# Kernel tuning notes

Hardware: AMD Instinct MI355X
Metric: run time of the kernel (lower is better)

Reference implementation:

```python
import jax, jax.numpy as jnp
import numpy as np

D_MODEL = 1024
D_HEAD = 512
EPS = 1e-6


def setup_inputs() -> dict:
    key = jax.random.key(0)
    ks = jax.random.split(key, 12)
    s = 0.02
    B, T = 8, 2048
    return {
        "x": jax.random.normal(ks[0], (B, T, D_MODEL), dtype=jnp.float32),
        "norm_w": jnp.ones((D_MODEL,), dtype=jnp.float32),
        "Wq": jax.random.normal(ks[1], (D_HEAD, D_MODEL), dtype=jnp.float32) * s,
        "Wk": jax.random.normal(ks[2], (D_HEAD, D_MODEL), dtype=jnp.float32) * s,
        "Wv": jax.random.normal(ks[3], (D_HEAD, D_MODEL), dtype=jnp.float32) * s,
        "wi_w": jax.random.normal(ks[4], (1, D_MODEL), dtype=jnp.float32) * s,
        "wi_b": jnp.zeros((1,), dtype=jnp.float32),
        "wf_w": jax.random.normal(ks[5], (1, D_MODEL), dtype=jnp.float32) * s,
        "wf_b": jnp.zeros((1,), dtype=jnp.float32),
        "Wo": jax.random.normal(ks[6], (D_HEAD, D_MODEL), dtype=jnp.float32) * s,
        "bo": jnp.zeros((D_HEAD,), dtype=jnp.float32),
        "Wout": jax.random.normal(ks[7], (D_MODEL, D_HEAD), dtype=jnp.float32) * s,
    }


def _forward(x, norm_w, Wq, Wk, Wv, wi_w, wi_b, wf_w, wf_b, Wo, bo, Wout):
    B, T, d_model = x.shape
    d = Wq.shape[0]
    scale = 1.0 / jnp.sqrt(jnp.asarray(d, x.dtype))

    # RMSNorm (pre-norm)
    normed = x * jax.lax.rsqrt(jnp.mean(x * x, axis=-1, keepdims=True) + EPS) * norm_w

    # Precompute all per-timestep projections (vectorized over T)
    q = jnp.einsum('btm,dm->btd', normed, Wq) * scale  # (B,T,d)
    k = jnp.einsum('btm,dm->btd', normed, Wk) * scale
    v = jnp.einsum('btm,dm->btd', normed, Wv)
    zi = jnp.einsum('btm,m->bt', normed, wi_w[0]) + wi_b[0]  # (B,T)
    zf = jnp.einsum('btm,m->bt', normed, wf_w[0]) + wf_b[0]
    o = jax.nn.sigmoid(jnp.einsum('btm,dm->btd', normed, Wo) + bo)  # (B,T,d)

    # Time-major for scan
    qT = jnp.moveaxis(q, 1, 0)
    kT = jnp.moveaxis(k, 1, 0)
    vT = jnp.moveaxis(v, 1, 0)
    ziT = jnp.moveaxis(zi, 1, 0)
    zfT = jnp.moveaxis(zf, 1, 0)
    oT = jnp.moveaxis(o, 1, 0)

    C0 = jnp.zeros((B, d, d), x.dtype)
    n0 = jnp.zeros((B, d), x.dtype)
    m0 = jnp.full((B,), -jnp.inf, x.dtype)

    def step(carry, inp):
        C, n, m = carry
        q_t, k_t, v_t, zi_t, zf_t, o_t = inp
        m_t = jnp.maximum(zf_t + m, zi_t)                      # (B,)
        i_p = jnp.exp(zi_t - m_t)
        f_p = jnp.exp(zf_t + m - m_t)
        C_t = f_p[:, None, None] * C + i_p[:, None, None] * (v_t[:, :, None] * k_t[:, None, :])
        n_t = f_p[:, None] * n + i_p[:, None] * k_t
        Cq = jnp.einsum('bij,bj->bi', C_t, q_t)                # (B,d)
        denom = jnp.maximum(jnp.abs(jnp.sum(n_t * q_t, axis=-1, keepdims=True)), 1.0)
        h = o_t * Cq / denom
        return (C_t, n_t, m_t), h

    (C_f, n_f, m_f), hT = jax.lax.scan(step, (C0, n0, m0), (qT, kT, vT, ziT, zfT, oT))
    h = jnp.moveaxis(hT, 0, 1)                                 # (B,T,d)
    out = x + jnp.einsum('btd,md->btm', h, Wout)
    return out


def reference(x, norm_w, Wq, Wk, Wv, wi_w, wi_b, wf_w, wf_b, Wo, bo, Wout):
    return _forward(x, norm_w, Wq, Wk, Wv, wi_w, wi_b, wf_w, wf_b, Wo, bo, Wout)
```

## Files before the change

### kernel.cpp

```cpp
#include <hip/hip_runtime.h>
#include <cstdint>
#include <cmath>

#define T_SEQ 2048
#define NBATCH 8
#define DM 1024
#define DH 512
#define MROWS (NBATCH * T_SEQ)
#define NC 16
#define CL 128

typedef short s8v __attribute__((ext_vector_type(8)));
typedef float f32x4 __attribute__((ext_vector_type(4)));

typedef unsigned int __attribute__((address_space(1))) uint_g;
typedef unsigned int __attribute__((address_space(3))) uint_l;

#define QKSCALE 0.044194173824159216f

__device__ __forceinline__ float b2f(unsigned short s) {
    union { unsigned u; float f; } c; c.u = ((unsigned)s) << 16; return c.f;
}
__device__ __forceinline__ unsigned short f2b(float f) {
    union { float f; unsigned u; } c; c.f = f;
    unsigned r = c.u + 0x7fffu + ((c.u >> 16) & 1u);
    return (unsigned short)(r >> 16);
}
__device__ __forceinline__ void gld_lds16(const void* g, void* l) {
    __builtin_amdgcn_global_load_lds((const uint_g*)g, (uint_l*)l, 16, 0, 0);
}

#define WAITV(N) asm volatile("s_waitcnt vmcnt(" #N ")" ::: "memory")
#define BARSYNC() do { asm volatile("" ::: "memory"); __builtin_amdgcn_s_barrier(); asm volatile("" ::: "memory"); } while (0)

__global__ __launch_bounds__(256) void norm_kernel(
    const float* __restrict__ x, const float* __restrict__ nw,
    const float* __restrict__ wi, const float* __restrict__ wf,
    const float* __restrict__ wib, const float* __restrict__ wfb,
    unsigned short* __restrict__ normed, float* __restrict__ zi, float* __restrict__ zf,
    const float* __restrict__ Wq, const float* __restrict__ Wk,
    const float* __restrict__ Wo, const float* __restrict__ Wv,
    const float* __restrict__ Wout,
    unsigned short* __restrict__ Wcat1, unsigned short* __restrict__ WvB,
    unsigned short* __restrict__ Woutb)
{
    int t = blockIdx.x, tid = threadIdx.x;
    float4 xv = ((const float4*)(x + (size_t)t * DM))[tid];
    float ss = xv.x * xv.x + xv.y * xv.y + xv.z * xv.z + xv.w * xv.w;
#pragma unroll
    for (int m = 1; m < 64; m <<= 1) ss += __shfl_xor(ss, m, 64);
    __shared__ float sred[4];
    __shared__ float sred2[8];
    if ((tid & 63) == 0) sred[tid >> 6] = ss;
    __syncthreads();
    ss = sred[0] + sred[1] + sred[2] + sred[3];
    float rstd = rsqrtf(ss * (1.0f / DM) + 1e-6f);
    float4 nwv = ((const float4*)nw)[tid];
    float n0 = xv.x * rstd * nwv.x, n1 = xv.y * rstd * nwv.y;
    float n2 = xv.z * rstd * nwv.z, n3 = xv.w * rstd * nwv.w;
    ushort4 pk;
    pk.x = f2b(n0); pk.y = f2b(n1); pk.z = f2b(n2); pk.w = f2b(n3);
    ((ushort4*)(normed + (size_t)t * DM))[tid] = pk;
    float4 wiv = ((const float4*)wi)[tid];
    float4 wfv = ((const float4*)wf)[tid];
    float pzi = n0 * wiv.x + n1 * wiv.y + n2 * wiv.z + n3 * wiv.w;
    float pzf = n0 * wfv.x + n1 * wfv.y + n2 * wfv.z + n3 * wfv.w;
#pragma unroll
    for (int m = 1; m < 64; m <<= 1) {
        pzi += __shfl_xor(pzi, m, 64);
        pzf += __shfl_xor(pzf, m, 64);
    }
    if ((tid & 63) == 0) { sred2[tid >> 6] = pzi; sred2[4 + (tid >> 6)] = pzf; }
    __syncthreads();
    if (tid == 0) {
        zi[t] = sred2[0] + sred2[1] + sred2[2] + sred2[3] + wib[0];
        zf[t] = sred2[4] + sred2[5] + sred2[6] + sred2[7] + wfb[0];
    }
    if (tid < 160) {
        int idx = blockIdx.x * 160 + tid;
        if (idx < 1572864) {
            int nrow = idx >> 10;
            float v;
            if      (nrow < 512)  v = Wq[idx];
            else if (nrow < 1024) v = Wk[idx - 512 * 1024];
            else                  v = Wo[idx - 1024 * 1024];
            Wcat1[idx] = f2b(v);
        } else if (idx < 2097152) {
            int j = idx - 1572864;
            WvB[j] = f2b(Wv[j]);
        } else {
            int j = idx - 2097152;
            Woutb[j] = f2b(Wout[j]);
        }
    }
}

__global__ __launch_bounds__(256, 4) void gemm_qkv_ms(
    const unsigned short* __restrict__ normed, const unsigned short* __restrict__ Wcat1,
    const unsigned short* __restrict__ WvB, int K,
    unsigned short* __restrict__ qko, const float* __restrict__ bo,
    unsigned short* __restrict__ vout,
    const float* __restrict__ zi, const float* __restrict__ zf,
    float* __restrict__ u, float* __restrict__ a)
{
    __shared__ unsigned short As[128 * 64];
    __shared__ unsigned short Bs[128 * 64];
    __shared__ float wt[4];
    int tid = threadIdx.x;

    if (blockIdx.x >= 2048) {
        int b = blockIdx.x - 2048, lane = tid & 63, wid = tid >> 6;
        size_t base = (size_t)b * T_SEQ + tid * 8;
        float z_f[8], z_i[8];
        *(float4*)&z_f[0] = *(const float4*)&zf[base];
        *(float4*)&z_f[4] = *(const float4*)&zf[base + 4];
        *(float4*)&z_i[0] = *(const float4*)&zi[base];
        *(float4*)&z_i[4] = *(const float4*)&zi[base + 4];
        float c8[8]; float run = 0.0f;
#pragma unroll
        for (int i = 0; i < 8; ++i) { run += z_f[i]; c8[i] = run; }
        float v = run;
#pragma unroll
        for (int d = 1; d < 64; d <<= 1) {
            float o = __shfl_up(v, d, 64);
            if (lane >= d) v += o;
        }
        if (lane == 63) wt[wid] = v;
        __syncthreads();
        float woff = 0.0f;
        for (int j = 0; j < wid; ++j) woff += wt[j];
        float excl = __shfl_up(v, 1, 64);
        if (lane == 0) excl = 0.0f;
        float pre = woff + excl;
        float uu[8];
#pragma unroll
        for (int i = 0; i < 8; ++i) uu[i] = z_i[i] - (pre + c8[i]);
        *(float4*)&u[base] = *(float4*)&uu[0];
        *(float4*)&u[base + 4] = *(float4*)&uu[4];
        __syncthreads();
        float m8[8]; float rm = -INFINITY;
#pragma unroll
        for (int i = 0; i < 8; ++i) { rm = fmaxf(rm, uu[i]); m8[i] = rm; }
        float mv = rm;
#pragma unroll
        for (int d = 1; d < 64; d <<= 1) {
            float o = __shfl_up(mv, d, 64);
            if (lane >= d) mv = fmaxf(mv, o);
        }
        if (lane == 63) wt[wid] = mv;
        __syncthreads();
        float moff = -INFINITY;
        for (int j = 0; j < wid; ++j) moff = fmaxf(moff, wt[j]);
        float mexcl = __shfl_up(mv, 1, 64);
        if (lane == 0) mexcl = -INFINITY;
        float mpre = fmaxf(moff, mexcl);
        float aa[8];
#pragma unroll
        for (int i = 0; i < 8; ++i) aa[i] = fmaxf(mpre, m8[i]);
        *(float4*)&a[base] = *(float4*)&aa[0];
        *(float4*)&a[base + 4] = *(float4*)&aa[4];
        return;
    }

    int l = tid & 63, w = tid >> 6;
    int wg = (blockIdx.x & 7) * 256 + (blockIdx.x >> 3);
    int job = (wg >= 1536) ? 1 : 0;
    const unsigned short* A;
    const unsigned short* Bw;
    int bm, bn;
    if (job == 0) { A = normed; Bw = Wcat1; bn = wg % 12; bm = wg / 12; }
    else          { int w2 = wg - 1536; A = WvB; Bw = normed; bm = w2 & 3; bn = w2 >> 2; }
    int wr = w >> 1, wc = w & 1;
    f32x4 acc[4][4] = {};
    const size_t abase = (size_t)(bm * 128) * K;
    const size_t bbase = (size_t)(bn * 128) * K;

    for (int ks = 0; ks < K; ks += 64) {
        __syncthreads();
#pragma unroll
        for (int i = 0; i < 4; ++i) {
            int off = (i * 256 + tid) * 8;
            int row = off >> 6, kc = off & 63;
            int kcs = kc ^ ((row & 7) << 3);
            gld_lds16(A + abase + (size_t)row * K + ks + kcs, &As[off]);
            gld_lds16(Bw + bbase + (size_t)row * K + ks + kcs, &Bs[off]);
        }
        __syncthreads();
#pragma unroll
        for (int kk = 0; kk < 2; ++kk) {
            int cbo = kk * 32 + (l >> 4) * 8;
            s8v af[4], bfv[4];
#pragma unroll
            for (int m = 0; m < 4; ++m) {
                int row = wr * 64 + m * 16 + (l & 15);
                af[m] = *(const s8v*)&As[row * 64 + (cbo ^ ((row & 7) << 3))];
            }
#pragma unroll
            for (int n = 0; n < 4; ++n) {
                int row = wc * 64 + n * 16 + (l & 15);
                bfv[n] = *(const s8v*)&Bs[row * 64 + (cbo ^ ((row & 7) << 3))];
            }
#pragma unroll
            for (int m = 0; m < 4; ++m)
#pragma unroll
                for (int n = 0; n < 4; ++n)
                    acc[m][n] = __builtin_amdgcn_mfma_f32_16x16x32_bf16(af[m], bfv[n], acc[m][n], 0, 0, 0);
        }
    }

    if (job == 0) {
#pragma unroll
        for (int m = 0; m < 4; ++m) {
#pragma unroll
            for (int n = 0; n < 4; ++n) {
                int col = bn * 128 + wc * 64 + n * 16 + (l & 15);
#pragma unroll
                for (int r = 0; r < 4; ++r) {
                    int row = bm * 128 + wr * 64 + m * 16 + (l >> 4) * 4 + r;
                    float v = acc[m][n][r];
                    if (col < 1024) v *= QKSCALE;
                    else {
                        float s = v + bo[col - 1024];
                        v = 1.0f / (1.0f + expf(-s));
                    }
                    qko[(size_t)row * 1536 + col] = f2b(v);
                }
            }
        }
    } else {
#pragma unroll
        for (int m = 0; m < 4; ++m) {
#pragma unroll
            for (int n = 0; n < 4; ++n) {
                int col = bn * 128 + wc * 64 + n * 16 + (l & 15);
#pragma unroll
                for (int r = 0; r < 4; ++r) {
                    int row = bm * 128 + wr * 64 + m * 16 + (l >> 4) * 4 + r;
                    vout[(size_t)row * MROWS + col] = f2b(acc[m][n][r]);
                }
            }
        }
    }
}

template <int EPI, int ORD>
__global__ __launch_bounds__(256, 4) void gemm_bt(
    const unsigned short* __restrict__ A, const unsigned short* __restrict__ Bw,
    int M, int N, int K, int ldo,
    unsigned short* __restrict__ outb, const float* __restrict__ bo,
    float* __restrict__ outf, const float* __restrict__ xres)
{
    __shared__ unsigned short As[128 * 64];
    __shared__ unsigned short Bs[128 * 64];
    int tid = threadIdx.x;
    int l = tid & 63, w = tid >> 6;
    int cpx = gridDim.x >> 3;
    int wg = (blockIdx.x & 7) * cpx + (blockIdx.x >> 3);
    int mb = M >> 7;
    int nb = N >> 7;
    int bm, bn;
    if (ORD == 0) { bm = wg % mb; bn = wg / mb; }
    else          { bn = wg % nb; bm = wg / nb; }
    int wr = w >> 1, wc = w & 1;
    f32x4 acc[4][4] = {};
    const size_t abase = (size_t)(bm * 128) * K;
    const size_t bbase = (size_t)(bn * 128) * K;

    for (int ks = 0; ks < K; ks += 64) {
        __syncthreads();
#pragma unroll
        for (int i = 0; i < 4; ++i) {
            int off = (i * 256 + tid) * 8;
            int row = off >> 6, kc = off & 63;
            int kcs = kc ^ ((row & 7) << 3);
            gld_lds16(A + abase + (size_t)row * K + ks + kcs, &As[off]);
            gld_lds16(Bw + bbase + (size_t)row * K + ks + kcs, &Bs[off]);
        }
        __syncthreads();
#pragma unroll
        for (int kk = 0; kk < 2; ++kk) {
            int cbo = kk * 32 + (l >> 4) * 8;
            s8v af[4], bfv[4];
#pragma unroll
            for (int m = 0; m < 4; ++m) {
                int row = wr * 64 + m * 16 + (l & 15);
                af[m] = *(const s8v*)&As[row * 64 + (cbo ^ ((row & 7) << 3))];
            }
#pragma unroll
            for (int n = 0; n < 4; ++n) {
                int row = wc * 64 + n * 16 + (l & 15);
                bfv[n] = *(const s8v*)&Bs[row * 64 + (cbo ^ ((row & 7) << 3))];
            }
#pragma unroll
            for (int m = 0; m < 4; ++m)
#pragma unroll
                for (int n = 0; n < 4; ++n)
                    acc[m][n] = __builtin_amdgcn_mfma_f32_16x16x32_bf16(af[m], bfv[n], acc[m][n], 0, 0, 0);
        }
    }

#pragma unroll
    for (int m = 0; m < 4; ++m) {
#pragma unroll
        for (int n = 0; n < 4; ++n) {
            int col = bn * 128 + wc * 64 + n * 16 + (l & 15);
#pragma unroll
            for (int r = 0; r < 4; ++r) {
                int row = bm * 128 + wr * 64 + m * 16 + (l >> 4) * 4 + r;
                float v = acc[m][n][r];
                if (EPI == 3) {
                    outb[(size_t)row * ldo + col] = f2b(v);
                } else {
                    size_t idx = (size_t)row * ldo + col;
                    outf[idx] = xres[idx] + v;
                }
            }
        }
    }
}

__global__ __launch_bounds__(256) void fusedA_kernel(
    const unsigned short* __restrict__ qko,
    const float* __restrict__ u, const float* __restrict__ a,
    unsigned short* __restrict__ stb, float* __restrict__ rowsum,
    unsigned short* __restrict__ kw, float* __restrict__ P, float* __restrict__ aE)
{
    __shared__ char smem[17920];
    int bid = blockIdx.x, tid = threadIdx.x;

    if (bid < 256) {
        unsigned short* Qs = (unsigned short*)smem;
        unsigned short* Ks = (unsigned short*)(smem + 4096);
        int b = bid & 7, c = (bid >> 3) & 15, th = bid >> 7;
        int l = tid & 63, wv = tid >> 6;
        size_t cb = (size_t)b * T_SEQ + c * CL;
        f32x4 acc[8] = {};
        for (int ks = 0; ks < 512; ks += 32) {
            __syncthreads();
            {
                int p = tid;
                int row = p >> 2, kc = (p & 3) * 8;
                gld_lds16(qko + (cb + th * 64 + row) * 1536 + ks + kc, &Qs[p * 8]);
#pragma unroll
                for (int rI = 0; rI < 2; ++rI) {
                    int pp = rI * 256 + tid;
                    int rw = pp >> 2, kk = (pp & 3) * 8;
                    gld_lds16(qko + (cb + rw) * 1536 + 512 + ks + kk, &Ks[pp * 8]);
                }
            }
            __syncthreads();
            s8v af = *(const s8v*)&Qs[(wv * 16 + (l & 15)) * 32 + (l >> 4) * 8];
#pragma unroll
            for (int n = 0; n < 8; ++n) {
                s8v bf = *(const s8v*)&Ks[(n * 16 + (l & 15)) * 32 + (l >> 4) * 8];
                acc[n] = __builtin_amdgcn_mfma_f32_16x16x32_bf16(af, bf, acc[n], 0, 0, 0);
            }
        }
        float rs[4] = {0.f, 0.f, 0.f, 0.f};
        size_t stbase = (size_t)(b * NC + c) * (CL * CL);
#pragma unroll
        for (int e = 0; e < 4; ++e) {
            int tl = th * 64 + wv * 16 + (l >> 4) * 4 + e;
            float a_t = a[cb + tl];
#pragma unroll
            for (int n = 0; n < 8; ++n) {
                int j = n * 16 + (l & 15);
                float val = (j <= tl) ? acc[n][e] * expf(u[cb + j] - a_t) : 0.0f;
                rs[e] += val;
                stb[stbase + (size_t)tl * CL + j] = f2b(val);
            }
        }
#pragma unroll
        for (int e = 0; e < 4; ++e) {
#pragma unroll
            for (int m = 1; m < 16; m <<= 1) rs[e] += __shfl_xor(rs[e], m, 64);
        }
        if ((l & 15) == 0) {
#pragma unroll
            for (int e = 0; e < 4; ++e)
                rowsum[cb + th * 64 + wv * 16 + (l >> 4) * 4 + e] = rs[e];
        }
    } else {
        unsigned short (*T)[136] = (unsigned short(*)[136])smem;
        float* w_l = (float*)(smem + 17408);
        int kb = bid - 256;
        int b = kb & 7, c = (kb >> 3) & 15, stt = kb >> 7;
        int s0 = stt * 64;
        size_t cb = (size_t)b * T_SEQ + c * CL;
        float a_e = a[cb + CL - 1];
        if (tid < CL) w_l[tid] = expf(u[cb + tid] - a_e);
        if (tid == 0 && stt == 0) aE[b * NC + c] = a_e;
#pragma unroll
        for (int it = 0; it < 4; ++it) {
            int flat = it * 256 + tid;
            int t = flat >> 3, g = flat & 7;
            s8v v = *(const s8v*)&qko[(cb + t) * 1536 + 512 + s0 + g * 8];
#pragma unroll
            for (int e = 0; e < 8; ++e) T[g * 8 + e][t] = (unsigned short)v[e];
        }
        __syncthreads();
        int s = tid >> 2, tg = tid & 3;
        float psum = 0.0f;
#pragma unroll
        for (int j = 0; j < 4; ++j) {
            int t0 = tg * 32 + j * 8;
            s8v kv = *(const s8v*)&T[s][t0];
            s8v kwv;
#pragma unroll
            for (int e = 0; e < 8; ++e) {
                float f = b2f((unsigned short)kv[e]) * w_l[t0 + e];
                kwv[e] = (short)f2b(f);
                psum += f;
            }
            *(s8v*)&kw[(size_t)(s0 + s) * MROWS + cb + t0] = kwv;
        }
        psum += __shfl_xor(psum, 1, 64);
        psum += __shfl_xor(psum, 2, 64);
        if (tg == 0) P[(size_t)(b * NC + c) * 512 + s0 + s] = psum;
    }
}

__global__ __launch_bounds__(256, 2) void cscan3_kernel(
    const unsigned short* __restrict__ kvT, const unsigned short* __restrict__ kw,
    const float* __restrict__ aE, unsigned short* __restrict__ chk,
    const unsigned short* __restrict__ qko, const float* __restrict__ P,
    const float* __restrict__ a, const float* __restrict__ rowsum,
    float* __restrict__ rdnm)
{
    __shared__ unsigned short Vs[2][64 * 128];
    __shared__ unsigned short Ks[2][64 * 128];
    int bid = blockIdx.x;
    int b = bid & 7, rt = (bid >> 3) & 7, st = bid >> 6;
    int r0 = rt * 64, s0 = st * 64;
    int tid = threadIdx.x, l = tid & 63;
    int w = tid >> 6, wr = w >> 1, wc = w & 1;
    size_t tb = (size_t)b * T_SEQ;
    int srow = tid >> 4, sg = tid & 15;
    f32x4 acc[2][2] = {};
    float a_prev = 0.0f;

#define CSTAGE(c, buf) do { \
        size_t cb_ = tb + (size_t)(c) * CL; \
        _Pragma("unroll") \
        for (int i = 0; i < 4; ++i) { \
            int row_ = i * 16 + srow; \
            int gs_ = sg ^ (row_ & 7); \
            gld_lds16(kvT + (size_t)(512 + r0 + row_) * MROWS + cb_ + gs_ * 8, \
                      &Vs[buf][(i * 256 + tid) * 8]); \
        } \
        _Pragma("unroll") \
        for (int i = 0; i < 4; ++i) { \
            int row_ = i * 16 + srow; \
            int gs_ = sg ^ (row_ & 7); \
            gld_lds16(kw + (size_t)(s0 + row_) * MROWS + cb_ + gs_ * 8, \
                      &Ks[buf][(i * 256 + tid) * 8]); \
        } } while (0)

    CSTAGE(0, 0);
    for (int c = 0; c < NC; ++c) {
        int cur = c & 1;
        if (c + 1 < NC) { CSTAGE(c + 1, cur ^ 1); WAITV(8); }
        else            { WAITV(0); }
        BARSYNC();
        float a_e = aE[b * NC + c];
        if (c > 0) {
            unsigned short* slot = chk + (size_t)(b * (NC - 1) + (c - 1)) * (512 * 512);
#pragma unroll
            for (int m = 0; m < 2; ++m)
#pragma unroll
                for (int n = 0; n < 2; ++n)
#pragma unroll
                    for (int e = 0; e < 4; ++e) {
                        int r = r0 + wr * 32 + m * 16 + (l >> 4) * 4 + e;
                        int s = s0 + wc * 32 + n * 16 + (l & 15);
                        slot[r * 512 + s] = f2b(acc[m][n][e]);
                    }
            float gam = expf(a_prev - a_e);
#pragma unroll
            for (int m = 0; m < 2; ++m)
#pragma unroll
                for (int n = 0; n < 2; ++n)
#pragma unroll
                    for (int e = 0; e < 4; ++e) acc[m][n][e] *= gam;
        }
#pragma unroll
        for (int ks = 0; ks < 4; ++ks) {
            s8v vf[2], kf[2];
#pragma unroll
            for (int m = 0; m < 2; ++m) {
                int row = wr * 32 + m * 16 + (l & 15);
                int gf = ks * 4 + (l >> 4);
                vf[m] = *(const s8v*)&Vs[cur][row * 128 + ((gf ^ (row & 7)) << 3)];
            }
#pragma unroll
            for (int n = 0; n < 2; ++n) {
                int row = wc * 32 + n * 16 + (l & 15);
                int gf = ks * 4 + (l >> 4);
                kf[n] = *(const s8v*)&Ks[cur][row * 128 + ((gf ^ (row & 7)) << 3)];
            }
#pragma unroll
            for (int m = 0; m < 2; ++m)
#pragma unroll
                for (int n = 0; n < 2; ++n)
                    acc[m][n] = __builtin_amdgcn_mfma_f32_16x16x32_bf16(vf[m], kf[n], acc[m][n], 0, 0, 0);
        }
        a_prev = a_e;
        BARSYNC();
    }
#undef CSTAGE

    {
        int wv = tid >> 6;
        int t0 = bid * 32 + wv * 8;
        int bt = t0 >> 11, ct = (t0 & 2047) >> 7;
        float nh[8] = {0, 0, 0, 0, 0, 0, 0, 0};
        float aprev = 0.0f;
        for (int cp = 0; cp < ct; ++cp) {
            float ae = aE[bt * NC + cp];
            float gam = (cp == 0) ? 0.0f : expf(aprev - ae);
            const float* Pp = P + (size_t)(bt * NC + cp) * 512 + l * 8;
            float4 p0 = *(const float4*)Pp;
            float4 p1 = *(const float4*)(Pp + 4);
#pragma unroll
            for (int e = 0; e < 8; ++e) nh[e] *= gam;
            nh[0] += p0.x; nh[1] += p0.y; nh[2] += p0.z; nh[3] += p0.w;
            nh[4] += p1.x; nh[5] += p1.y; nh[6] += p1.z; nh[7] += p1.w;
            aprev = ae;
        }
        float aeprev = (ct > 0) ? aE[bt * NC + ct - 1] : 0.0f;
        for (int tt = 0; tt < 8; ++tt) {
            int tc = t0 + tt;
            s8v qv = *(const s8v*)(qko + (size_t)tc * 1536 + l * 8);
            float nq = 0.0f;
#pragma unroll
            for (int e = 0; e < 8; ++e) nq += b2f((unsigned short)qv[e]) * nh[e];
#pragma unroll
            for (int m = 1; m < 64; m <<= 1) nq += __shfl_xor(nq, m, 64);
            if (l == 0) {
                float beta = (ct == 0) ? 0.0f : expf(aeprev - a[tc]);
                rdnm[tc] = 1.0f / fmaxf(fabsf(beta * nq + rowsum[tc]), 1.0f);
            }
        }
    }
}

__global__ __launch_bounds__(512) void hout_kernel(
    const unsigned short* __restrict__ qko, const unsigned short* __restrict__ kvT,
    const unsigned short* __restrict__ st, const unsigned short* __restrict__ chk,
    const float* __restrict__ a, const float* __restrict__ aE,
    const float* __restrict__ rdnm, unsigned short* __restrict__ g)
{
    int bid = blockIdx.x;
    int b = bid & 7, cc = bid >> 3;
    int c = cc >> 1, rh = cc & 1;
    int tid = threadIdx.x, l = tid & 63, wv = tid >> 6;
    int mq = wv & 3;
    int rr = (wv >> 2) * 128 + rh * 256;
    size_t cb = (size_t)b * T_SEQ + c * CL;
    f32x4 acc[2][8] = {};

    if (c > 0) {
        const unsigned short* slot = chk + (size_t)(b * (NC - 1) + (c - 1)) * (512 * 512);
#pragma unroll
        for (int ks = 0; ks < 16; ++ks) {
            s8v aq[2];
#pragma unroll
            for (int mf = 0; mf < 2; ++mf)
                aq[mf] = *(const s8v*)&qko[(cb + mq * 32 + mf * 16 + (l & 15)) * 1536 + ks * 32 + (l >> 4) * 8];
#pragma unroll
            for (int n = 0; n < 8; ++n) {
                s8v bc = *(const s8v*)&slot[(size_t)(rr + n * 16 + (l & 15)) * 512 + ks * 32 + (l >> 4) * 8];
                acc[0][n] = __builtin_amdgcn_mfma_f32_16x16x32_bf16(aq[0], bc, acc[0][n], 0, 0, 0);
                acc[1][n] = __builtin_amdgcn_mfma_f32_16x16x32_bf16(aq[1], bc, acc[1][n], 0, 0, 0);
            }
        }
        float aprev = aE[b * NC + c - 1];
#pragma unroll
        for (int mf = 0; mf < 2; ++mf)
#pragma unroll
            for (int e = 0; e < 4; ++e) {
                int t = mq * 32 + mf * 16 + (l >> 4) * 4 + e;
                float bta = expf(aprev - a[cb + t]);
#pragma unroll
                for (int n = 0; n < 8; ++n) acc[mf][n][e] *= bta;
            }
    }
    const unsigned short* stp = st + (size_t)(b * NC + c) * (CL * CL);
#pragma unroll
    for (int ks = 0; ks < 4; ++ks) {
        s8v aq[2];
#pragma unroll
        for (int mf = 0; mf < 2; ++mf)
            aq[mf] = *(const s8v*)&stp[(size_t)(mq * 32 + mf * 16 + (l & 15)) * CL + ks * 32 + (l >> 4) * 8];
#pragma unroll
        for (int n = 0; n < 8; ++n) {
            s8v bv = *(const s8v*)&kvT[(size_t)(512 + rr + n * 16 + (l & 15)) * MROWS + cb + ks * 32 + (l >> 4) * 8];
            acc[0][n] = __builtin_amdgcn_mfma_f32_16x16x32_bf16(aq[0], bv, acc[0][n], 0, 0, 0);
            acc[1][n] = __builtin_amdgcn_mfma_f32_16x16x32_bf16(aq[1], bv, acc[1][n], 0, 0, 0);
        }
    }
#pragma unroll
    for (int mf = 0; mf < 2; ++mf)
#pragma unroll
        for (int e = 0; e < 4; ++e) {
            int t = mq * 32 + mf * 16 + (l >> 4) * 4 + e;
            float rd = rdnm[cb + t];
#pragma unroll
            for (int n = 0; n < 8; ++n) {
                int r = rr + n * 16 + (l & 15);
                float ov = b2f(qko[(cb + t) * 1536 + 1024 + r]);
                g[(cb + t) * DH + r] = f2b(ov * acc[mf][n][e] * rd);
            }
        }
}

extern "C" void kernel_launch(void* const* d_in, const int* in_sizes, int n_in,
                              void* d_out, int out_size, void* d_ws, size_t ws_size,
                              hipStream_t stream)
{
    (void)in_sizes; (void)n_in; (void)out_size; (void)ws_size;
    const float* x    = (const float*)d_in[0];
    const float* nw   = (const float*)d_in[1];
    const float* Wq   = (const float*)d_in[2];
    const float* Wk   = (const float*)d_in[3];
    const float* Wv   = (const float*)d_in[4];
    const float* wi   = (const float*)d_in[5];
    const float* wib  = (const float*)d_in[6];
    const float* wf   = (const float*)d_in[7];
    const float* wfb  = (const float*)d_in[8];
    const float* Wo   = (const float*)d_in[9];
    const float* bo   = (const float*)d_in[10];
    const float* Wout = (const float*)d_in[11];
    float* out = (float*)d_out;

    char* ws = (char*)d_ws;
    unsigned short* qko    = (unsigned short*)ws;
    unsigned short* kvT    = (unsigned short*)(ws + 50331648);
    unsigned short* normed = (unsigned short*)(ws + 83886080);
    unsigned short* g      = normed;
    unsigned short* kw     = (unsigned short*)(ws + 100663296);
    float* Pbuf   = (float*)(ws + 117440512);
    float* aE     = (float*)(ws + 117964800);
    unsigned short* Wcat1  = (unsigned short*)(ws + 117440512);
    unsigned short* WvB    = (unsigned short*)(ws + 120586240);
    unsigned short* Woutb  = (unsigned short*)(ws + 122683392);
    float* zi     = (float*)(ws + 123731968);
    float* zf     = zi + MROWS;
    float* uarr   = zf + MROWS;
    float* aarr   = uarr + MROWS;
    float* rowsum = aarr + MROWS;
    float* rdnm   = rowsum + MROWS;

    unsigned short* chk   = (unsigned short*)d_out;
    unsigned short* stbuf = (unsigned short*)((char*)d_out + 62914560);

    norm_kernel    <<<MROWS, 256, 0, stream>>>(x, nw, wi, wf, wib, wfb, normed, zi, zf,
                                               Wq, Wk, Wo, Wv, Wout, Wcat1, WvB, Woutb);
    gemm_qkv_ms    <<<2056, 256, 0, stream>>>(normed, Wcat1, WvB, DM, qko, bo,
                                              kvT + (size_t)512 * MROWS, zi, zf, uarr, aarr);
    fusedA_kernel  <<<1280, 256, 0, stream>>>(qko, uarr, aarr, stbuf, rowsum, kw, Pbuf, aE);
    cscan3_kernel  <<<512, 256, 0, stream>>>(kvT, kw, aE, chk, qko, Pbuf, aarr, rowsum, rdnm);
    hout_kernel    <<<256, 512, 0, stream>>>(qko, kvT, stbuf, chk, aarr, aE, rdnm, g);
    gemm_bt<1, 1>  <<<128 * 8, 256, 0, stream>>>(g, Woutb, MROWS, DM, DH, DM, nullptr, nullptr, out, x);
}
```

Measured before the change: 273.3 us.

## Stage chunk-state and V tiles through swizzled LDS with double buffering in hout

The hout kernel previously had every wave read its B operands (chunk state matrix and V columns) straight from global memory, so the four waves sharing a row group fetched the same data redundantly. It now loads 256x64 B tiles cooperatively into XOR-swizzled shared memory with direct global-to-LDS loads, double-buffered so the next K-slice loads while MFMAs consume the current one. This cuts global/L2 traffic and uncoalesced loads in exchange for 64KB of LDS per block and two barriers per stage.

```diff
diff --git a/kernel.cpp b/kernel.cpp
--- a/kernel.cpp
+++ b/kernel.cpp
@@ -544,36 +544,60 @@
     }
 }
 
-__global__ __launch_bounds__(512) void hout_kernel(
+__global__ __launch_bounds__(512) void hout2_kernel(
     const unsigned short* __restrict__ qko, const unsigned short* __restrict__ kvT,
     const unsigned short* __restrict__ st, const unsigned short* __restrict__ chk,
     const float* __restrict__ a, const float* __restrict__ aE,
     const float* __restrict__ rdnm, unsigned short* __restrict__ g)
 {
+    __shared__ unsigned short Bsh[2][256 * 64];
     int bid = blockIdx.x;
     int b = bid & 7, cc = bid >> 3;
     int c = cc >> 1, rh = cc & 1;
     int tid = threadIdx.x, l = tid & 63, wv = tid >> 6;
-    int mq = wv & 3;
-    int rr = (wv >> 2) * 128 + rh * 256;
+    int mq = wv & 3, rg = wv >> 2;
+    int rr = rg * 128 + rh * 256;
+    int R0 = rh * 256;
     size_t cb = (size_t)b * T_SEQ + c * CL;
     f32x4 acc[2][8] = {};
 
+    int srow7 = tid >> 3;
+    int sgc = tid & 7;
+
     if (c > 0) {
         const unsigned short* slot = chk + (size_t)(b * (NC - 1) + (c - 1)) * (512 * 512);
-#pragma unroll
-        for (int ks = 0; ks < 16; ++ks) {
-            s8v aq[2];
-#pragma unroll
-            for (int mf = 0; mf < 2; ++mf)
-                aq[mf] = *(const s8v*)&qko[(cb + mq * 32 + mf * 16 + (l & 15)) * 1536 + ks * 32 + (l >> 4) * 8];
-#pragma unroll
-            for (int n = 0; n < 8; ++n) {
-                s8v bc = *(const s8v*)&slot[(size_t)(rr + n * 16 + (l & 15)) * 512 + ks * 32 + (l >> 4) * 8];
-                acc[0][n] = __builtin_amdgcn_mfma_f32_16x16x32_bf16(aq[0], bc, acc[0][n], 0, 0, 0);
-                acc[1][n] = __builtin_amdgcn_mfma_f32_16x16x32_bf16(aq[1], bc, acc[1][n], 0, 0, 0);
-            }
-        }
+#define HSTG_C(ksb, buf) do { \
+        _Pragma("unroll") \
+        for (int i = 0; i < 4; ++i) { \
+            int row_ = i * 64 + srow7; \
+            int gs_ = sgc ^ (row_ & 7); \
+            gld_lds16(slot + (size_t)(R0 + row_) * 512 + (ksb) * 64 + gs_ * 8, \
+                      &Bsh[buf][(i * 512 + tid) * 8]); \
+        } } while (0)
+        HSTG_C(0, 0);
+        for (int s = 0; s < 8; ++s) {
+            int cur = s & 1;
+            if (s + 1 < 8) { HSTG_C(s + 1, cur ^ 1); WAITV(4); }
+            else           { WAITV(0); }
+            BARSYNC();
+#pragma unroll
+            for (int kk = 0; kk < 2; ++kk) {
+                s8v aq[2];
+#pragma unroll
+                for (int mf = 0; mf < 2; ++mf)
+                    aq[mf] = *(const s8v*)&qko[(cb + mq * 32 + mf * 16 + (l & 15)) * 1536 + s * 64 + kk * 32 + (l >> 4) * 8];
+#pragma unroll
+                for (int n = 0; n < 8; ++n) {
+                    int row = rg * 128 + n * 16 + (l & 15);
+                    int gr = (kk * 4 + (l >> 4)) ^ (row & 7);
+                    s8v bc = *(const s8v*)&Bsh[cur][row * 64 + gr * 8];
+                    acc[0][n] = __builtin_amdgcn_mfma_f32_16x16x32_bf16(aq[0], bc, acc[0][n], 0, 0, 0);
+                    acc[1][n] = __builtin_amdgcn_mfma_f32_16x16x32_bf16(aq[1], bc, acc[1][n], 0, 0, 0);
+                }
+            }
+            BARSYNC();
+        }
+#undef HSTG_C
         float aprev = aE[b * NC + c - 1];
 #pragma unroll
         for (int mf = 0; mf < 2; ++mf)
@@ -585,20 +609,40 @@
                 for (int n = 0; n < 8; ++n) acc[mf][n][e] *= bta;
             }
     }
+
     const unsigned short* stp = st + (size_t)(b * NC + c) * (CL * CL);
-#pragma unroll
-    for (int ks = 0; ks < 4; ++ks) {
-        s8v aq[2];
-#pragma unroll
-        for (int mf = 0; mf < 2; ++mf)
-            aq[mf] = *(const s8v*)&stp[(size_t)(mq * 32 + mf * 16 + (l & 15)) * CL + ks * 32 + (l >> 4) * 8];
-#pragma unroll
-        for (int n = 0; n < 8; ++n) {
-            s8v bv = *(const s8v*)&kvT[(size_t)(512 + rr + n * 16 + (l & 15)) * MROWS + cb + ks * 32 + (l >> 4) * 8];
-            acc[0][n] = __builtin_amdgcn_mfma_f32_16x16x32_bf16(aq[0], bv, acc[0][n], 0, 0, 0);
-            acc[1][n] = __builtin_amdgcn_mfma_f32_16x16x32_bf16(aq[1], bv, acc[1][n], 0, 0, 0);
-        }
-    }
+#define HSTG_V(vsb, buf) do { \
+        _Pragma("unroll") \
+        for (int i = 0; i < 4; ++i) { \
+            int row_ = i * 64 + srow7; \
+            int gs_ = sgc ^ (row_ & 7); \
+            gld_lds16(kvT + (size_t)(512 + R0 + row_) * MROWS + cb + (vsb) * 64 + gs_ * 8, \
+                      &Bsh[buf][(i * 512 + tid) * 8]); \
+        } } while (0)
+    HSTG_V(0, 0);
+    for (int s = 0; s < 2; ++s) {
+        if (s + 1 < 2) { HSTG_V(1, 1); WAITV(4); }
+        else           { WAITV(0); }
+        BARSYNC();
+#pragma unroll
+        for (int kk = 0; kk < 2; ++kk) {
+            s8v aq[2];
+#pragma unroll
+            for (int mf = 0; mf < 2; ++mf)
+                aq[mf] = *(const s8v*)&stp[(size_t)(mq * 32 + mf * 16 + (l & 15)) * CL + s * 64 + kk * 32 + (l >> 4) * 8];
+#pragma unroll
+            for (int n = 0; n < 8; ++n) {
+                int row = rg * 128 + n * 16 + (l & 15);
+                int gr = (kk * 4 + (l >> 4)) ^ (row & 7);
+                s8v bv = *(const s8v*)&Bsh[s][row * 64 + gr * 8];
+                acc[0][n] = __builtin_amdgcn_mfma_f32_16x16x32_bf16(aq[0], bv, acc[0][n], 0, 0, 0);
+                acc[1][n] = __builtin_amdgcn_mfma_f32_16x16x32_bf16(aq[1], bv, acc[1][n], 0, 0, 0);
+            }
+        }
+        BARSYNC();
+    }
+#undef HSTG_V
+
 #pragma unroll
     for (int mf = 0; mf < 2; ++mf)
 #pragma unroll
@@ -660,6 +704,6 @@
                                               kvT + (size_t)512 * MROWS, zi, zf, uarr, aarr);
     fusedA_kernel  <<<1280, 256, 0, stream>>>(qko, uarr, aarr, stbuf, rowsum, kw, Pbuf, aE);
     cscan3_kernel  <<<512, 256, 0, stream>>>(kvT, kw, aE, chk, qko, Pbuf, aarr, rowsum, rdnm);
-    hout_kernel    <<<256, 512, 0, stream>>>(qko, kvT, stbuf, chk, aarr, aE, rdnm, g);
+    hout2_kernel   <<<256, 512, 0, stream>>>(qko, kvT, stbuf, chk, aarr, aE, rdnm, g);
     gemm_bt<1, 1>  <<<128 * 8, 256, 0, stream>>>(g, Woutb, MROWS, DM, DH, DM, nullptr, nullptr, out, x);
 }
```

After: 243.6 us, median of 3. 1.12x faster.
